# Optimization experiments

Measured on AMD Instinct MI355X. Metric: run time of the kernel, lower is better.

## Reference

```python
import jax, jax.numpy as jnp
import numpy as np

N_NODES = 50000
N_EDGES = 800000
N_GRAPHS = 512
IN_DIM = 128
HID = 64


def setup_inputs() -> dict:
    key = jax.random.key(0)
    ks = jax.random.split(key, 12)
    x = jax.random.normal(ks[0], (N_NODES, IN_DIM), dtype=jnp.float32)
    edge_index = jax.random.randint(ks[1], (2, N_EDGES), 0, N_NODES, dtype=jnp.int64)
    batch = jnp.sort(jax.random.randint(ks[2], (N_NODES,), 0, N_GRAPHS, dtype=jnp.int64))

    def lin(k, fan_in, fan_out):
        # torch Linear default init: U(-1/sqrt(fan_in), 1/sqrt(fan_in)); stored as [in, out]
        bound = 1.0 / np.sqrt(fan_in)
        return jax.random.uniform(k, (fan_in, fan_out), minval=-bound, maxval=bound, dtype=jnp.float32)

    W1_1 = lin(ks[3], IN_DIM, HID)
    W2_1 = lin(ks[4], IN_DIM, HID)
    W1_2 = lin(ks[5], HID, HID)
    W2_2 = lin(ks[6], HID, HID)
    W1_3 = lin(ks[7], HID, HID)
    W2_3 = lin(ks[8], HID, HID)
    cW1 = lin(ks[9], HID, HID)
    cb1 = jnp.zeros((HID,), dtype=jnp.float32)
    cW2 = lin(ks[10], HID, 1)
    cb2 = jnp.zeros((1,), dtype=jnp.float32)
    return {"x": x, "edge_index": edge_index, "batch": batch,
            "W1_1": W1_1, "W2_1": W2_1, "W1_2": W1_2, "W2_2": W2_2,
            "W1_3": W1_3, "W2_3": W2_3, "cW1": cW1, "cb1": cb1,
            "cW2": cW2, "cb2": cb2}


def _gnn_layer(x, src, dst, W1, W2):
    # f(v) = relu( x[v] @ W1 + sum_{u in N(v)} x[u] @ W2 )
    self_part = x @ W1                      # [N, out]
    msg = x[src] @ W2                       # gather + matmul: [E, out]
    neigh = jax.ops.segment_sum(msg, dst, num_segments=N_NODES)  # scatter-add
    return jax.nn.relu(self_part + neigh)


def reference(x, edge_index, batch, W1_1, W2_1, W1_2, W2_2, W1_3, W2_3, cW1, cb1, cW2, cb2):
    src, dst = edge_index[0], edge_index[1]  # PyG source_to_target flow
    h = _gnn_layer(x, src, dst, W1_1, W2_1)
    h = _gnn_layer(h, src, dst, W1_2, W2_2)
    h = _gnn_layer(h, src, dst, W1_3, W2_3)
    # global_mean_pool over graph segments
    sums = jax.ops.segment_sum(h, batch, num_segments=N_GRAPHS)      # [G, HID]
    counts = jax.ops.segment_sum(jnp.ones((h.shape[0],), h.dtype), batch, num_segments=N_GRAPHS)
    pooled = sums / jnp.maximum(counts, 1.0)[:, None]
    # classifier MLP
    hcls = jax.nn.relu(pooled @ cW1 + cb1)
    return hcls @ cW2 + cb2                  # [G, 1]
```

## Files before the change

### kernel.cpp

```cpp
#include <hip/hip_runtime.h>


#define NSLOT 62
#define CAPB  4608

typedef __attribute__((ext_vector_type(8))) short short8;
typedef __attribute__((ext_vector_type(4))) float floatx4;
typedef __attribute__((ext_vector_type(2))) float floatx2;

__device__ __forceinline__ unsigned short f2bf(float f) {
    union { float f; unsigned u; } v; v.f = f;
    unsigned r = v.u + 0x7FFF + ((v.u >> 16) & 1);
    return (unsigned short)(r >> 16);
}

__device__ __forceinline__ unsigned char f2fp8(float f) {
    int v = __builtin_amdgcn_cvt_pk_fp8_f32(f, 0.f, 0, false);
    return (unsigned char)(v & 0xff);
}

__device__ __forceinline__ void fp8x8fma(float* t, uint2 w, float s) {
    floatx2 p;
    p = __builtin_amdgcn_cvt_pk_f32_fp8(w.x, false);
    t[0] = fmaf(p[0], s, t[0]); t[1] = fmaf(p[1], s, t[1]);
    p = __builtin_amdgcn_cvt_pk_f32_fp8(w.x, true);
    t[2] = fmaf(p[0], s, t[2]); t[3] = fmaf(p[1], s, t[3]);
    p = __builtin_amdgcn_cvt_pk_f32_fp8(w.y, false);
    t[4] = fmaf(p[0], s, t[4]); t[5] = fmaf(p[1], s, t[5]);
    p = __builtin_amdgcn_cvt_pk_f32_fp8(w.y, true);
    t[6] = fmaf(p[0], s, t[6]); t[7] = fmaf(p[1], s, t[7]);
}

__device__ __forceinline__ void bf8unpack(uint4 w, float* s) {
    s[0] = __uint_as_float(w.x << 16);
    s[1] = __uint_as_float(w.x & 0xffff0000u);
    s[2] = __uint_as_float(w.y << 16);
    s[3] = __uint_as_float(w.y & 0xffff0000u);
    s[4] = __uint_as_float(w.z << 16);
    s[5] = __uint_as_float(w.z & 0xffff0000u);
    s[6] = __uint_as_float(w.w << 16);
    s[7] = __uint_as_float(w.w & 0xffff0000u);
}

__device__ __forceinline__ void gather_row(
    const unsigned char* __restrict__ M, const unsigned short* __restrict__ csrx,
    int node, int cg, float* acc8, int N)
{
    const int nodeC = node < N ? node : 0;
    const uint4* bv = (const uint4*)(csrx + (size_t)nodeC * 64);
    uint4 q0 = bv[0], q1 = bv[1], q2 = bv[2], q3 = bv[3];
    int c = node < N ? (int)q0.x : 0;
    if (c > NSLOT) c = NSLOT;

    unsigned ia[16], ib[14];
    ia[0]  = q0.y & 0xffff; ia[1]  = q0.y >> 16;
    ia[2]  = q0.z & 0xffff; ia[3]  = q0.z >> 16;
    ia[4]  = q0.w & 0xffff; ia[5]  = q0.w >> 16;
    ia[6]  = q1.x & 0xffff; ia[7]  = q1.x >> 16;
    ia[8]  = q1.y & 0xffff; ia[9]  = q1.y >> 16;
    ia[10] = q1.z & 0xffff; ia[11] = q1.z >> 16;
    ia[12] = q1.w & 0xffff; ia[13] = q1.w >> 16;
    ia[14] = q2.x & 0xffff; ia[15] = q2.x >> 16;
    ib[0]  = q2.y & 0xffff; ib[1]  = q2.y >> 16;
    ib[2]  = q2.z & 0xffff; ib[3]  = q2.z >> 16;
    ib[4]  = q2.w & 0xffff; ib[5]  = q2.w >> 16;
    ib[6]  = q3.x & 0xffff; ib[7]  = q3.x >> 16;
    ib[8]  = q3.y & 0xffff; ib[9]  = q3.y >> 16;
    ib[10] = q3.z & 0xffff; ib[11] = q3.z >> 16;
    ib[12] = q3.w & 0xffff; ib[13] = q3.w >> 16;

#pragma unroll
    for (int j = 0; j < 16; ++j) if (j >= c) ia[j] = 0;
#pragma unroll
    for (int j = 0; j < 14; ++j) if (16 + j >= c) ib[j] = 0;

    uint2 wa[16];
#pragma unroll
    for (int j = 0; j < 16; ++j)
        wa[j] = *(const uint2*)&M[(size_t)ia[j] * 64 + cg * 8];
    uint2 wb[14];
#pragma unroll
    for (int j = 0; j < 14; ++j)
        wb[j] = *(const uint2*)&M[(size_t)ib[j] * 64 + cg * 8];

    float a[8], b[8];
#pragma unroll
    for (int j = 0; j < 8; ++j) { a[j] = 0.f; b[j] = 0.f; }
#pragma unroll
    for (int j = 0; j < 16; ++j)
        fp8x8fma((j & 1) ? b : a, wa[j], (j < c) ? 1.f : 0.f);
#pragma unroll
    for (int j = 0; j < 14; ++j)
        fp8x8fma((j & 1) ? b : a, wb[j], (16 + j < c) ? 1.f : 0.f);

    for (int base = 30; base < c; base += 8) {
        uint4 q = bv[4 + ((base - 30) >> 3)];
        unsigned id2[8];
        id2[0] = q.x & 0xffff; id2[1] = q.x >> 16;
        id2[2] = q.y & 0xffff; id2[3] = q.y >> 16;
        id2[4] = q.z & 0xffff; id2[5] = q.z >> 16;
        id2[6] = q.w & 0xffff; id2[7] = q.w >> 16;
#pragma unroll
        for (int j = 0; j < 8; ++j)
            if (base + j >= c) id2[j] = 0;
        uint2 w2[8];
#pragma unroll
        for (int j = 0; j < 8; ++j)
            w2[j] = *(const uint2*)&M[(size_t)id2[j] * 64 + cg * 8];
#pragma unroll
        for (int j = 0; j < 8; ++j)
            fp8x8fma((j & 1) ? b : a, w2[j], (base + j < c) ? 1.f : 0.f);
    }
#pragma unroll
    for (int j = 0; j < 8; ++j) acc8[j] = a[j] + b[j];
}


__device__ __forceinline__ void mm1_body(
    const float* __restrict__ Xraw,
    const float* __restrict__ W1, const float* __restrict__ W2,
    unsigned short* __restrict__ S, unsigned char* __restrict__ M,
    int N, int blk)
{
    __shared__ __align__(16) unsigned short Xs[64][72];
    __shared__ __align__(16) unsigned short Ws[128][72];
    const int tid  = threadIdx.x;
    const int lane = tid & 63;
    const int wv   = tid >> 6;
    const int lrow = lane & 15;
    const int quad = lane >> 4;
    const int row0 = blk * 64;

    floatx4 acc[8];
#pragma unroll
    for (int i = 0; i < 8; ++i) acc[i] = (floatx4){0.f, 0.f, 0.f, 0.f};

    const int xr  = tid >> 2;
    const int xk  = (tid & 3) * 16;
    const int gxr = row0 + xr;

    for (int ko = 0; ko < 128; ko += 64) {
#pragma unroll
        for (int q = 0; q < 4; ++q) {
            float4 v = make_float4(0.f, 0.f, 0.f, 0.f);
            if (gxr < N) v = *(const float4*)&Xraw[(size_t)gxr * 128 + ko + xk + q * 4];
            ushort4 p;
            p.x = f2bf(v.x); p.y = f2bf(v.y); p.z = f2bf(v.z); p.w = f2bf(v.w);
            *(ushort4*)&Xs[xr][xk + q * 4] = p;
        }
#pragma unroll
        for (int i = 0; i < 2; ++i) {
            int s  = tid + i * 256;
            int k0 = (s & 15) * 4;
            int c0 = (s >> 4) * 4;
            float wr[4][4];
#pragma unroll
            for (int r = 0; r < 4; ++r) {
                int gk = ko + k0 + r;
                float4 t4 = (c0 < 64) ? *(const float4*)&W1[(size_t)gk * 64 + c0]
                                      : *(const float4*)&W2[(size_t)gk * 64 + (c0 - 64)];
                wr[r][0] = t4.x; wr[r][1] = t4.y; wr[r][2] = t4.z; wr[r][3] = t4.w;
            }
#pragma unroll
            for (int j = 0; j < 4; ++j) {
                ushort4 col;
                col.x = f2bf(wr[0][j]); col.y = f2bf(wr[1][j]);
                col.z = f2bf(wr[2][j]); col.w = f2bf(wr[3][j]);
                *(ushort4*)&Ws[c0 + j][k0] = col;
            }
        }
        __syncthreads();

#pragma unroll
        for (int kc = 0; kc < 2; ++kc) {
            int kofs = kc * 32 + quad * 8;
            short8 a = *(const short8*)&Xs[wv * 16 + lrow][kofs];
#pragma unroll
            for (int ct = 0; ct < 8; ++ct) {
                short8 b = *(const short8*)&Ws[ct * 16 + lrow][kofs];
                acc[ct] = __builtin_amdgcn_mfma_f32_16x16x32_bf16(a, b, acc[ct], 0, 0, 0);
            }
        }
        __syncthreads();
    }

    const int orow = row0 + wv * 16 + quad * 4;
#pragma unroll
    for (int ct = 0; ct < 8; ++ct) {
        int col = ct * 16 + lrow;
#pragma unroll
        for (int r = 0; r < 4; ++r) {
            int gr = orow + r;
            if (gr < N) {
                if (ct < 4) S[(size_t)gr * 64 + col] = f2bf(acc[ct][r]);
                else        M[(size_t)gr * 64 + (col - 64)] = f2fp8(acc[ct][r]);
            }
        }
    }
}

__device__ __forceinline__ void bucketize_body(
    const int* __restrict__ ei, unsigned* __restrict__ sorted,
    int* __restrict__ gcur, int E, int NB, int bid, int stride)
{
    __shared__ int lhist[256];
    __shared__ int lcur[256];
    const int tid = threadIdx.x;

    int base = bid * 256 + tid;
    int e[8], d[8], s[8];
    bool v[8];
#pragma unroll
    for (int j = 0; j < 8; ++j) {
        e[j] = base + j * stride;
        v[j] = e[j] < E;
        if (v[j]) {
            d[j] = ei[E + e[j]];
            s[j] = ei[e[j]];
        }
    }

    lhist[tid] = 0;
    __syncthreads();
#pragma unroll
    for (int j = 0; j < 8; ++j)
        if (v[j]) atomicAdd(&lhist[d[j] >> 8], 1);
    __syncthreads();
    if (tid < NB && lhist[tid] > 0)
        lcur[tid] = atomicAdd(&gcur[tid], lhist[tid]);
    __syncthreads();
#pragma unroll
    for (int j = 0; j < 8; ++j) {
        if (v[j]) {
            int b   = d[j] >> 8;
            int pos = atomicAdd(&lcur[b], 1);
            if (pos < CAPB)
                sorted[(size_t)b * CAPB + pos] =
                    (unsigned)s[j] | ((unsigned)(d[j] & 255) << 16);
        }
    }
}

__global__ __launch_bounds__(256) void mm1_bucket_kernel(
    const float* __restrict__ Xraw,
    const float* __restrict__ W1, const float* __restrict__ W2,
    unsigned short* __restrict__ S, unsigned char* __restrict__ M, int N,
    const int* __restrict__ ei, unsigned* __restrict__ sorted,
    int* __restrict__ gcur, int E, int NB, int edgeBlocks)
{
    if ((int)blockIdx.x < edgeBlocks) {
        bucketize_body(ei, sorted, gcur, E, NB, blockIdx.x, edgeBlocks * 256);
    } else {
        mm1_body(Xraw, W1, W2, S, M, N, (int)blockIdx.x - edgeBlocks);
    }
}

__global__ __launch_bounds__(256) void bucket_csr_kernel(
    const unsigned* __restrict__ sorted, const int* __restrict__ gcur,
    unsigned short* __restrict__ csrx, int N)
{
    __shared__ unsigned short rows[256][NSLOT];
    __shared__ int cnt[256];
    const int b   = blockIdx.x;
    const int tid = threadIdx.x;

    cnt[tid] = 0;
    __syncthreads();

    int cb = gcur[b];
    if (cb > CAPB) cb = CAPB;
    const unsigned* src = sorted + (size_t)b * CAPB;
    for (int i = tid; i < cb; i += 256) {
        unsigned p = src[i];
        int ln = (p >> 16) & 255;
        int pos = atomicAdd(&cnt[ln], 1);
        if (pos < NSLOT) rows[ln][pos] = (unsigned short)(p & 0xffff);
    }
    __syncthreads();

    int r  = tid >> 3;
    int ch = tid & 7;
    for (int it = 0; it < 8; ++it, r += 32) {
        int gn = b * 256 + r;
        if (gn < N) {
            const unsigned short* sl = rows[r];
            uint4 v;
            if (ch == 0) {
                v.x = (unsigned)cnt[r];
                v.y = sl[0] | ((unsigned)sl[1] << 16);
                v.z = sl[2] | ((unsigned)sl[3] << 16);
                v.w = sl[4] | ((unsigned)sl[5] << 16);
            } else {
                int s0 = ch * 8 - 2;
                v.x = sl[s0]     | ((unsigned)sl[s0 + 1] << 16);
                v.y = sl[s0 + 2] | ((unsigned)sl[s0 + 3] << 16);
                v.z = sl[s0 + 4] | ((unsigned)sl[s0 + 5] << 16);
                v.w = sl[s0 + 6] | ((unsigned)sl[s0 + 7] << 16);
            }
            *(uint4*)(csrx + (size_t)gn * 64 + ch * 8) = v;
        }
    }
}

__global__ __launch_bounds__(256) void mm_gather_kernel(
    const unsigned short* __restrict__ Sprev, const unsigned char* __restrict__ Mprev,
    const unsigned short* __restrict__ csrx,
    const float* __restrict__ W1, const float* __restrict__ W2,
    unsigned short* __restrict__ Sout, unsigned char* __restrict__ Mout, int N)
{
    __shared__ __align__(16) unsigned short Xs[32][72];
    __shared__ __align__(16) unsigned short Ws[128][72];
    const int tid  = threadIdx.x;
    const int lane = tid & 63;
    const int wv   = tid >> 6;
    const int lrow = lane & 15;
    const int quad = lane >> 4;
    const int row0 = blockIdx.x * 32;
    const int slot = tid >> 3;
    const int cg   = tid & 7;

#pragma unroll
    for (int i = 0; i < 2; ++i) {
        int s  = tid + i * 256;
        int k0 = (s & 15) * 4;
        int c0 = (s >> 4) * 4;
        float wr[4][4];
#pragma unroll
        for (int r = 0; r < 4; ++r) {
            int gk = k0 + r;
            float4 t4 = (c0 < 64) ? *(const float4*)&W1[(size_t)gk * 64 + c0]
                                  : *(const float4*)&W2[(size_t)gk * 64 + (c0 - 64)];
            wr[r][0] = t4.x; wr[r][1] = t4.y; wr[r][2] = t4.z; wr[r][3] = t4.w;
        }
#pragma unroll
        for (int j = 0; j < 4; ++j) {
            ushort4 col;
            col.x = f2bf(wr[0][j]); col.y = f2bf(wr[1][j]);
            col.z = f2bf(wr[2][j]); col.w = f2bf(wr[3][j]);
            *(ushort4*)&Ws[c0 + j][k0] = col;
        }
    }

    {
        int node = row0 + slot;
        float g8[8];
        gather_row(Mprev, csrx, node, cg, g8, N);
        float r8[8];
        if (node < N) {
            uint4 h = *(const uint4*)&Sprev[(size_t)node * 64 + cg * 8];
            float s8[8];
            bf8unpack(h, s8);
#pragma unroll
            for (int j = 0; j < 8; ++j) r8[j] = fmaxf(g8[j] + s8[j], 0.f);
        } else {
#pragma unroll
            for (int j = 0; j < 8; ++j) r8[j] = 0.f;
        }
        ushort4 p0, p1;
        p0.x = f2bf(r8[0]); p0.y = f2bf(r8[1]); p0.z = f2bf(r8[2]); p0.w = f2bf(r8[3]);
        p1.x = f2bf(r8[4]); p1.y = f2bf(r8[5]); p1.z = f2bf(r8[6]); p1.w = f2bf(r8[7]);
        *(ushort4*)&Xs[slot][cg * 8]     = p0;
        *(ushort4*)&Xs[slot][cg * 8 + 4] = p1;
    }
    __syncthreads();

    const int rowgrp   = wv >> 1;
    const int colhalf  = wv & 1;
    floatx4 acc[4];
#pragma unroll
    for (int i = 0; i < 4; ++i) acc[i] = (floatx4){0.f, 0.f, 0.f, 0.f};
#pragma unroll
    for (int kc = 0; kc < 2; ++kc) {
        int kofs = kc * 32 + quad * 8;
        short8 a = *(const short8*)&Xs[rowgrp * 16 + lrow][kofs];
#pragma unroll
        for (int ctl = 0; ctl < 4; ++ctl) {
            int ct = colhalf * 4 + ctl;
            short8 b = *(const short8*)&Ws[ct * 16 + lrow][kofs];
            acc[ctl] = __builtin_amdgcn_mfma_f32_16x16x32_bf16(a, b, acc[ctl], 0, 0, 0);
        }
    }

    const int orow = row0 + rowgrp * 16 + quad * 4;
#pragma unroll
    for (int ctl = 0; ctl < 4; ++ctl) {
        int col = (colhalf * 4 + ctl) * 16 + lrow;
#pragma unroll
        for (int r = 0; r < 4; ++r) {
            int gr = orow + r;
            if (gr < N) {
                if (colhalf == 0) Sout[(size_t)gr * 64 + col] = f2bf(acc[ctl][r]);
                else              Mout[(size_t)gr * 64 + (col - 64)] = f2fp8(acc[ctl][r]);
            }
        }
    }
}

__global__ __launch_bounds__(512) void pool_gather_cls_kernel(
    const unsigned short* __restrict__ S, const unsigned char* __restrict__ M,
    const unsigned short* __restrict__ csrx,
    const int* __restrict__ batch,
    const float* __restrict__ cW1, const float* __restrict__ cb1,
    const float* __restrict__ cW2, const float* __restrict__ cb2,
    float* __restrict__ out, int N)
{
    int g  = blockIdx.x;
    int t  = threadIdx.x;
    int wv = t >> 6;
    int lane = t & 63;
    int eg = lane >> 3;
    int cg = lane & 7;
    int slot = wv * 8 + eg;

    int lo = 0, hi = N;
    while (lo < hi) { int mid = (lo + hi) >> 1; if (batch[mid] < g) lo = mid + 1; else hi = mid; }
    int start = lo;
    hi = N;
    while (lo < hi) { int mid = (lo + hi) >> 1; if (batch[mid] < g + 1) lo = mid + 1; else hi = mid; }
    int end = lo;

    float p8[8];
#pragma unroll
    for (int j = 0; j < 8; ++j) p8[j] = 0.f;

    for (int r = start + slot; r < end; r += 64) {
        float g8[8];
        gather_row(M, csrx, r, cg, g8, N);
        uint4 h = *(const uint4*)&S[(size_t)r * 64 + cg * 8];
        float s8[8];
        bf8unpack(h, s8);
#pragma unroll
        for (int j = 0; j < 8; ++j) p8[j] += fmaxf(g8[j] + s8[j], 0.f);
    }

    __shared__ float part[64][64];
    __shared__ float pooled[64];
#pragma unroll
    for (int j = 0; j < 8; ++j) part[slot][cg * 8 + j] = p8[j];
    __syncthreads();

    if (t < 64) {
        float s = 0.f;
#pragma unroll 8
        for (int k = 0; k < 64; ++k) s += part[k][t];
        float c_ = (float)((end - start) > 0 ? (end - start) : 1);
        pooled[t] = s / c_;
    }
    __syncthreads();
    if (t < 64) {
        float a = cb1[t];
#pragma unroll 8
        for (int k = 0; k < 64; ++k) a += pooled[k] * cW1[k * 64 + t];
        a = fmaxf(a, 0.f);
        float o = a * cW2[t];
#pragma unroll
        for (int off_ = 32; off_ > 0; off_ >>= 1) o += __shfl_down(o, off_);
        if (t == 0) out[g] = o + cb2[0];
    }
}

extern "C" void kernel_launch(void* const* d_in, const int* in_sizes, int n_in,
                              void* d_out, int out_size, void* d_ws, size_t ws_size,
                              hipStream_t stream)
{
    const float* x     = (const float*)d_in[0];
    const int*   ei    = (const int*)d_in[1];
    const int*   batch = (const int*)d_in[2];
    const float* W1_1  = (const float*)d_in[3];
    const float* W2_1  = (const float*)d_in[4];
    const float* W1_2  = (const float*)d_in[5];
    const float* W2_2  = (const float*)d_in[6];
    const float* W1_3  = (const float*)d_in[7];
    const float* W2_3  = (const float*)d_in[8];
    const float* cW1   = (const float*)d_in[9];
    const float* cb1   = (const float*)d_in[10];
    const float* cW2   = (const float*)d_in[11];
    const float* cb2   = (const float*)d_in[12];
    float* out = (float*)d_out;

    const int N = in_sizes[0] / 128;
    const int E = in_sizes[1] / 2;
    const int G = out_size;
    const int NB = (N + 255) >> 8;

    unsigned char*  MA     = (unsigned char*)d_ws;
    unsigned short* SA     = (unsigned short*)(MA + (size_t)N * 64);
    unsigned short* csrx   = SA + (size_t)N * 64;
    unsigned char*  MB     = (unsigned char*)(csrx + (size_t)N * 64);
    unsigned short* SB     = (unsigned short*)(MB + (size_t)N * 64);
    unsigned*       sorted = (unsigned*)(SB + (size_t)N * 64);
    int*            gcur   = (int*)(sorted + (size_t)NB * CAPB);

    const int mmGrid  = (N + 63) / 64;
    const int gGrid   = (N + 31) / 32;
    const int edgeBlocks = (E + 2047) / 2048;

    (void)hipMemsetAsync(gcur, 0, (size_t)NB * sizeof(int), stream);

    mm1_bucket_kernel<<<edgeBlocks + mmGrid, 256, 0, stream>>>(
        x, W1_1, W2_1, SA, MA, N, ei, sorted, gcur, E, NB, edgeBlocks);
    bucket_csr_kernel<<<NB, 256, 0, stream>>>(sorted, gcur, csrx, N);
    mm_gather_kernel<<<gGrid, 256, 0, stream>>>(
        SA, MA, csrx, W1_2, W2_2, SB, MB, N);
    mm_gather_kernel<<<gGrid, 256, 0, stream>>>(
        SB, MB, csrx, W1_3, W2_3, SA, MA, N);
    pool_gather_cls_kernel<<<G, 512, 0, stream>>>(
        SA, MA, csrx, batch, cW1, cb1, cW2, cb2, out, N);
}
```

Before: 180.7 us.

## Split pooling across two blocks per graph and prefetch gather table slices

The final pooling kernel now runs two blocks per graph, each taking alternate 64-row chunks. The blocks combine partial sums with float atomics into a zeroed buffer, and a separate small classifier kernel does the mean and MLP. The gather kernels also issue a dummy strided load of the fp8 message table at entry to warm L2 before the dependent gathers. The aim is more parallelism in the tail kernel and fewer cache misses, at the cost of an extra launch, atomics, and wasted warm-up loads.

```diff
diff --git a/kernel.cpp b/kernel.cpp
--- a/kernel.cpp
+++ b/kernel.cpp
@@ -40,6 +40,16 @@
     s[5] = __uint_as_float(w.z & 0xffff0000u);
     s[6] = __uint_as_float(w.w << 16);
     s[7] = __uint_as_float(w.w & 0xffff0000u);
+}
+
+__device__ __forceinline__ void warm_M(
+    const unsigned char* __restrict__ M, int N, int bid, int tid, int slice)
+{
+    const size_t mb = (size_t)N * 64;
+    size_t span = (size_t)slice;
+    size_t off = ((size_t)(bid >> 3) * span) % (mb > span ? mb - span : 1);
+    uint2 d = *(const uint2*)(M + off + (size_t)tid * 64);
+    asm volatile("" :: "v"(d.x), "v"(d.y));
 }
 
 __device__ __forceinline__ void gather_row(
@@ -319,6 +329,8 @@
     const int slot = tid >> 3;
     const int cg   = tid & 7;
 
+    warm_M(Mprev, N, blockIdx.x, tid, 16384);
+
 #pragma unroll
     for (int i = 0; i < 2; ++i) {
         int s  = tid + i * 256;
@@ -396,21 +408,21 @@
     }
 }
 
-__global__ __launch_bounds__(512) void pool_gather_cls_kernel(
+__global__ __launch_bounds__(512) void pool_act_kernel(
     const unsigned short* __restrict__ S, const unsigned char* __restrict__ M,
     const unsigned short* __restrict__ csrx,
-    const int* __restrict__ batch,
-    const float* __restrict__ cW1, const float* __restrict__ cb1,
-    const float* __restrict__ cW2, const float* __restrict__ cb2,
-    float* __restrict__ out, int N)
-{
-    int g  = blockIdx.x;
-    int t  = threadIdx.x;
-    int wv = t >> 6;
+    const int* __restrict__ batch, float* __restrict__ pooled32, int N)
+{
+    int g    = blockIdx.x >> 1;
+    int half = blockIdx.x & 1;
+    int t    = threadIdx.x;
+    int wv   = t >> 6;
     int lane = t & 63;
-    int eg = lane >> 3;
-    int cg = lane & 7;
+    int eg   = lane >> 3;
+    int cg   = lane & 7;
     int slot = wv * 8 + eg;
+
+    warm_M(M, N, blockIdx.x, t, 32768);
 
     int lo = 0, hi = N;
     while (lo < hi) { int mid = (lo + hi) >> 1; if (batch[mid] < g) lo = mid + 1; else hi = mid; }
@@ -423,7 +435,7 @@
 #pragma unroll
     for (int j = 0; j < 8; ++j) p8[j] = 0.f;
 
-    for (int r = start + slot; r < end; r += 64) {
+    for (int r = start + half * 64 + slot; r < end; r += 128) {
         float g8[8];
         gather_row(M, csrx, r, cg, g8, N);
         uint4 h = *(const uint4*)&S[(size_t)r * 64 + cg * 8];
@@ -434,7 +446,6 @@
     }
 
     __shared__ float part[64][64];
-    __shared__ float pooled[64];
 #pragma unroll
     for (int j = 0; j < 8; ++j) part[slot][cg * 8 + j] = p8[j];
     __syncthreads();
@@ -443,20 +454,39 @@
         float s = 0.f;
 #pragma unroll 8
         for (int k = 0; k < 64; ++k) s += part[k][t];
-        float c_ = (float)((end - start) > 0 ? (end - start) : 1);
-        pooled[t] = s / c_;
-    }
-    __syncthreads();
-    if (t < 64) {
-        float a = cb1[t];
+        atomicAdd(&pooled32[(size_t)g * 64 + t], s);
+    }
+}
+
+__global__ __launch_bounds__(64) void cls_kernel(
+    const float* __restrict__ pooled32, const int* __restrict__ batch,
+    const float* __restrict__ cW1, const float* __restrict__ cb1,
+    const float* __restrict__ cW2, const float* __restrict__ cb2,
+    float* __restrict__ out, int N)
+{
+    int g = blockIdx.x;
+    int t = threadIdx.x;
+
+    int lo = 0, hi = N;
+    while (lo < hi) { int mid = (lo + hi) >> 1; if (batch[mid] < g) lo = mid + 1; else hi = mid; }
+    int start = lo;
+    hi = N;
+    while (lo < hi) { int mid = (lo + hi) >> 1; if (batch[mid] < g + 1) lo = mid + 1; else hi = mid; }
+    int cnt = lo - start;
+    float inv = 1.f / (float)(cnt > 0 ? cnt : 1);
+
+    __shared__ float pl[64];
+    pl[t] = pooled32[(size_t)g * 64 + t] * inv;
+    __syncthreads();
+
+    float a = cb1[t];
 #pragma unroll 8
-        for (int k = 0; k < 64; ++k) a += pooled[k] * cW1[k * 64 + t];
-        a = fmaxf(a, 0.f);
-        float o = a * cW2[t];
-#pragma unroll
-        for (int off_ = 32; off_ > 0; off_ >>= 1) o += __shfl_down(o, off_);
-        if (t == 0) out[g] = o + cb2[0];
-    }
+    for (int k = 0; k < 64; ++k) a += pl[k] * cW1[k * 64 + t];
+    a = fmaxf(a, 0.f);
+    float o = a * cW2[t];
+#pragma unroll
+    for (int off_ = 32; off_ > 0; off_ >>= 1) o += __shfl_down(o, off_);
+    if (t == 0) out[g] = o + cb2[0];
 }
 
 extern "C" void kernel_launch(void* const* d_in, const int* in_sizes, int n_in,
@@ -490,12 +520,14 @@
     unsigned short* SB     = (unsigned short*)(MB + (size_t)N * 64);
     unsigned*       sorted = (unsigned*)(SB + (size_t)N * 64);
     int*            gcur   = (int*)(sorted + (size_t)NB * CAPB);
+    float*          pooled32 = (float*)(gcur + NB);
 
     const int mmGrid  = (N + 63) / 64;
     const int gGrid   = (N + 31) / 32;
     const int edgeBlocks = (E + 2047) / 2048;
 
-    (void)hipMemsetAsync(gcur, 0, (size_t)NB * sizeof(int), stream);
+    (void)hipMemsetAsync(gcur, 0,
+        (size_t)NB * sizeof(int) + (size_t)G * 64 * sizeof(float), stream);
 
     mm1_bucket_kernel<<<edgeBlocks + mmGrid, 256, 0, stream>>>(
         x, W1_1, W2_1, SA, MA, N, ei, sorted, gcur, E, NB, edgeBlocks);
@@ -504,6 +536,8 @@
         SA, MA, csrx, W1_2, W2_2, SB, MB, N);
     mm_gather_kernel<<<gGrid, 256, 0, stream>>>(
         SB, MB, csrx, W1_3, W2_3, SA, MA, N);
-    pool_gather_cls_kernel<<<G, 512, 0, stream>>>(
-        SA, MA, csrx, batch, cW1, cb1, cW2, cb2, out, N);
-}
+    pool_act_kernel<<<G * 2, 512, 0, stream>>>(
+        SA, MA, csrx, batch, pooled32, N);
+    cls_kernel<<<G, 64, 0, stream>>>(
+        pooled32, batch, cW1, cb1, cW2, cb2, out, N);
+}
```

Measured after the change: 202.4 us. 1.12x slower.
